# Performance work log

Measured on AMD Instinct MI355X. Metric: run time of the kernel, lower is better.

The kernel has to match this reference:

```python
import jax, jax.numpy as jnp
import numpy as np

H = 768  # sparse grid height
W = 768  # sparse grid width
N = 200000  # active sites
CIN = 256
CB = 64


def setup_inputs() -> dict:
    key = jax.random.key(0)
    ks = jax.random.split(key, 11)
    rng = np.random.default_rng(0)
    # unique active-site linear coordinates on the HxW grid
    coords = jnp.asarray(np.sort(rng.choice(H * W, N, replace=False)).astype(np.int64))
    feats = jax.random.normal(ks[0], (N, CIN), jnp.float32)
    w1 = jax.random.normal(ks[1], (CIN, CB), jnp.float32) / np.float32(np.sqrt(CIN))
    w2 = jax.random.normal(ks[2], (9, CB, CB), jnp.float32) / np.float32(np.sqrt(9 * CB))
    w3 = jax.random.normal(ks[3], (CB, CIN), jnp.float32) / np.float32(np.sqrt(CB))
    s1 = jax.random.uniform(ks[4], (CB,), jnp.float32, 0.5, 1.5)
    b1 = jax.random.normal(ks[5], (CB,), jnp.float32) * 0.1
    s2 = jax.random.uniform(ks[6], (CB,), jnp.float32, 0.5, 1.5)
    b2 = jax.random.normal(ks[7], (CB,), jnp.float32) * 0.1
    s3 = jax.random.uniform(ks[8], (CIN,), jnp.float32, 0.5, 1.5)
    b3 = jax.random.normal(ks[9], (CIN,), jnp.float32) * 0.1
    return dict(feats=feats, coords=coords, w1=w1, w2=w2, w3=w3,
                s1=s1, b1=b1, s2=s2, b2=b2, s3=s3, b3=b3)


def sparse_conv3x3(feats, coords, w2):
    # active-site sparse 3x3 conv: gather valid neighbors, matmul per tap, accumulate
    idx_map = jnp.full((H * W,), -1, jnp.int32).at[coords].set(
        jnp.arange(N, dtype=jnp.int32))
    y, x = coords // W, coords % W
    out = jnp.zeros((N, w2.shape[2]), feats.dtype)
    k = 0
    for dy in (-1, 0, 1):
        for dx in (-1, 0, 1):
            ny, nx = y + dy, x + dx
            inb = (ny >= 0) & (ny < H) & (nx >= 0) & (nx < W)
            lin = jnp.clip(ny, 0, H - 1) * W + jnp.clip(nx, 0, W - 1)
            r = idx_map[lin]
            ok = inb & (r >= 0)
            g = jnp.where(ok[:, None], feats[jnp.maximum(r, 0)], 0.0)
            out = out + g @ w2[k]
            k += 1
    return out


def reference(feats, coords, w1, w2, w3, s1, b1, s2, b2, s3, b3):
    identity = feats
    out = jax.nn.relu((feats @ w1) * s1 + b1)            # conv1 1x1 + bn1 + relu
    out = jax.nn.relu(sparse_conv3x3(out, coords, w2) * s2 + b2)  # conv2 3x3 + bn2 + relu
    out = (out @ w3) * s3 + b3                            # conv3 1x1 + bn3
    return jax.nn.relu(out + identity)                    # residual + relu
```

## Files before the change

kernel.cpp:

```cpp
#include <hip/hip_runtime.h>
#include <hip/hip_bf16.h>
#include <stdint.h>

#define HH 768
#define WW 768
#define NN 200000
#define CI 256
#define CB 64

typedef __attribute__((ext_vector_type(8))) __bf16 bf16x8;
typedef __attribute__((ext_vector_type(4))) float f32x4;

__device__ inline unsigned short f2bf(float f) {
    union { float f; unsigned int i; } v; v.f = f;
    unsigned int r = v.i + 0x7FFF + ((v.i >> 16) & 1);
    return (unsigned short)(r >> 16);
}
__device__ inline f32x4 mfma16(bf16x8 a, bf16x8 b, f32x4 c) {
    return __builtin_amdgcn_mfma_f32_16x16x32_bf16(a, b, c, 0, 0, 0);
}
__device__ inline bf16x8 ldfrag(const unsigned short* p) {
    return *(const bf16x8*)p;
}
__device__ inline bf16x8 ldfrag_f32(const float* p) {
    float4 f0 = *(const float4*)(p);
    float4 f1 = *(const float4*)(p + 4);
    bf16x8 a;
    a[0] = (__bf16)f0.x; a[1] = (__bf16)f0.y; a[2] = (__bf16)f0.z; a[3] = (__bf16)f0.w;
    a[4] = (__bf16)f1.x; a[5] = (__bf16)f1.y; a[6] = (__bf16)f1.z; a[7] = (__bf16)f1.w;
    return a;
}


__global__ void k_scatter(const int* __restrict__ coords, int* __restrict__ idx_map) {
    int i = blockIdx.x * 256 + threadIdx.x;
    if (i < NN) idx_map[coords[i]] = i;
}

__global__ void k_prepw(const float* __restrict__ w1,
                        const float* __restrict__ w2,
                        const float* __restrict__ w3,
                        unsigned short* __restrict__ w1t,
                        unsigned short* __restrict__ w2t,
                        unsigned short* __restrict__ w3t) {
    int tid = blockIdx.x * 256 + threadIdx.x;
    int stride = gridDim.x * 256;
    for (int i = tid; i < CI * CB; i += stride) {
        int k = i / CB, n = i % CB;
        w1t[n * CI + k] = f2bf(w1[i]);
    }
    for (int i = tid; i < 9 * CB * CB; i += stride) {
        int t = i / (CB * CB), rem = i % (CB * CB);
        int k = rem / CB, n = rem % CB;
        w2t[t * CB * CB + n * CB + k] = f2bf(w2[i]);
    }
    for (int i = tid; i < CB * CI; i += stride) {
        int k = i / CI, n = i % CI;
        w3t[n * CB + k] = f2bf(w3[i]);
    }
}


__global__ __launch_bounds__(256) void k_gemm1(const float* __restrict__ feats,
                                               const unsigned short* __restrict__ w1t,
                                               const float* __restrict__ s1,
                                               const float* __restrict__ b1,
                                               unsigned short* __restrict__ out1) {
    const int wave = threadIdx.x >> 6;
    const int lane = threadIdx.x & 63;
    const int m = lane & 15;
    const int quad = lane >> 4;
    const int row0 = blockIdx.x * 64 + wave * 16;
    const int row = row0 + m;

    f32x4 acc[4];
#pragma unroll
    for (int t = 0; t < 4; ++t) acc[t] = (f32x4){0.f, 0.f, 0.f, 0.f};

    const float* arow = feats + row * CI + quad * 8;
#pragma unroll
    for (int ks = 0; ks < CI / 32; ++ks) {
        bf16x8 a = ldfrag_f32(arow + ks * 32);
#pragma unroll
        for (int t = 0; t < 4; ++t) {
            bf16x8 b = ldfrag(w1t + (t * 16 + m) * CI + quad * 8 + ks * 32);
            acc[t] = mfma16(a, b, acc[t]);
        }
    }

#pragma unroll
    for (int t = 0; t < 4; ++t) {
        int col = t * 16 + m;
        float sc = s1[col], bi = b1[col];
#pragma unroll
        for (int r = 0; r < 4; ++r) {
            int orow = row0 + quad * 4 + r;
            float v = acc[t][r] * sc + bi;
            v = v > 0.f ? v : 0.f;
            out1[orow * CB + col] = f2bf(v);
        }
    }
}


__global__ __launch_bounds__(256) void k_conv(const unsigned short* __restrict__ out1,
                                              const unsigned short* __restrict__ w2t,
                                              const int* __restrict__ coords,
                                              const int* __restrict__ idx_map,
                                              const float* __restrict__ s2,
                                              const float* __restrict__ b2,
                                              unsigned short* __restrict__ out2) {
    const int wave = threadIdx.x >> 6;
    const int lane = threadIdx.x & 63;
    const int m = lane & 15;
    const int quad = lane >> 4;
    const int row0 = blockIdx.x * 64 + wave * 16;
    const int row = row0 + m;

    const int c = coords[row];
    const int y = c / WW, x = c - y * WW;

    f32x4 acc[4];
#pragma unroll
    for (int t = 0; t < 4; ++t) acc[t] = (f32x4){0.f, 0.f, 0.f, 0.f};

#pragma unroll
    for (int t = 0; t < 9; ++t) {
        const int dy = t / 3 - 1, dx = t % 3 - 1;
        const int ny = y + dy, nx = x + dx;
        int r = -1;
        if (ny >= 0 && ny < HH && nx >= 0 && nx < WW) r = idx_map[ny * WW + nx];
#pragma unroll
        for (int ks = 0; ks < 2; ++ks) {
            bf16x8 a;
#pragma unroll
            for (int j = 0; j < 8; ++j) a[j] = (__bf16)0.0f;
            if (r >= 0) a = ldfrag(out1 + r * CB + quad * 8 + ks * 32);
#pragma unroll
            for (int nt = 0; nt < 4; ++nt) {
                bf16x8 b = ldfrag(w2t + t * CB * CB + (nt * 16 + m) * CB + quad * 8 + ks * 32);
                acc[nt] = mfma16(a, b, acc[nt]);
            }
        }
    }

#pragma unroll
    for (int nt = 0; nt < 4; ++nt) {
        int col = nt * 16 + m;
        float sc = s2[col], bi = b2[col];
#pragma unroll
        for (int r = 0; r < 4; ++r) {
            int orow = row0 + quad * 4 + r;
            float v = acc[nt][r] * sc + bi;
            v = v > 0.f ? v : 0.f;
            out2[orow * CB + col] = f2bf(v);
        }
    }
}


__global__ __launch_bounds__(256) void k_gemm3(const unsigned short* __restrict__ out2,
                                               const unsigned short* __restrict__ w3t,
                                               const float* __restrict__ s3,
                                               const float* __restrict__ b3,
                                               const float* __restrict__ feats,
                                               float* __restrict__ out) {
    const int wave = threadIdx.x >> 6;
    const int lane = threadIdx.x & 63;
    const int m = lane & 15;
    const int quad = lane >> 4;
    const int row0 = blockIdx.x * 64 + wave * 16;
    const int row = row0 + m;

    f32x4 acc[16];
#pragma unroll
    for (int t = 0; t < 16; ++t) acc[t] = (f32x4){0.f, 0.f, 0.f, 0.f};

    bf16x8 a0 = ldfrag(out2 + row * CB + quad * 8);
    bf16x8 a1 = ldfrag(out2 + row * CB + quad * 8 + 32);
#pragma unroll
    for (int nt = 0; nt < 16; ++nt) {
        const unsigned short* bp = w3t + (nt * 16 + m) * CB + quad * 8;
        acc[nt] = mfma16(a0, ldfrag(bp), acc[nt]);
        acc[nt] = mfma16(a1, ldfrag(bp + 32), acc[nt]);
    }

#pragma unroll
    for (int nt = 0; nt < 16; ++nt) {
        int col = nt * 16 + m;
        float sc = s3[col], bi = b3[col];
#pragma unroll
        for (int r = 0; r < 4; ++r) {
            int orow = row0 + quad * 4 + r;
            float v = acc[nt][r] * sc + bi + feats[orow * CI + col];
            v = v > 0.f ? v : 0.f;
            out[orow * CI + col] = v;
        }
    }
}


extern "C" void kernel_launch(void* const* d_in, const int* in_sizes, int n_in,
                              void* d_out, int out_size, void* d_ws, size_t ws_size,
                              hipStream_t stream) {
    const float* feats = (const float*)d_in[0];
    const int* coords = (const int*)d_in[1];
    const float* w1 = (const float*)d_in[2];
    const float* w2 = (const float*)d_in[3];
    const float* w3 = (const float*)d_in[4];
    const float* s1 = (const float*)d_in[5];
    const float* b1 = (const float*)d_in[6];
    const float* s2 = (const float*)d_in[7];
    const float* b2 = (const float*)d_in[8];
    const float* s3 = (const float*)d_in[9];
    const float* b3 = (const float*)d_in[10];
    float* out = (float*)d_out;

    char* ws = (char*)d_ws;
    int* idx_map        = (int*)(ws + 0);
    unsigned short* w1t = (unsigned short*)(ws + 2359296);
    unsigned short* w2t = (unsigned short*)(ws + 2392064);
    unsigned short* w3t = (unsigned short*)(ws + 2465792);
    unsigned short* out1= (unsigned short*)(ws + 2498560);
    unsigned short* out2= (unsigned short*)(ws + 28098560);

    hipMemsetAsync(idx_map, 0xFF, (size_t)HH * WW * 4, stream);
    k_scatter<<<(NN + 255) / 256, 256, 0, stream>>>(coords, idx_map);
    k_prepw<<<64, 256, 0, stream>>>(w1, w2, w3, w1t, w2t, w3t);
    k_gemm1<<<NN / 64, 256, 0, stream>>>(feats, w1t, s1, b1, out1);
    k_conv<<<NN / 64, 256, 0, stream>>>(out1, w2t, coords, idx_map, s2, b2, out2);
    k_gemm3<<<NN / 64, 256, 0, stream>>>(out2, w3t, s3, b3, feats, out);
}
```

Baseline: 591.7 us.

## Register-block all three GEMM stages to 64x64 wave tiles, stage conv neighbors in LDS

Each wave now computes a 64-row by 64-column tile: four M-subtiles by four N-subtiles of MFMA accumulators. Each weight fragment load is therefore reused across four row blocks instead of one, in gemm1, conv and gemm3. The conv kernel first computes all nine neighbor indices per row into shared memory. It then gathers from a zeroed dummy row instead of branching on missing neighbors. gemm3 splits the 256 output columns across the four waves so they share the same activation rows. The trade-off is much higher register pressure, capped by launch bounds of 2 blocks per CU, and fewer waves for gemm1 and conv.

```diff
diff --git a/kernel.cpp b/kernel.cpp
--- a/kernel.cpp
+++ b/kernel.cpp
@@ -61,142 +61,186 @@
 }
 
 
-__global__ __launch_bounds__(256) void k_gemm1(const float* __restrict__ feats,
-                                               const unsigned short* __restrict__ w1t,
-                                               const float* __restrict__ s1,
-                                               const float* __restrict__ b1,
-                                               unsigned short* __restrict__ out1) {
+__global__ __launch_bounds__(256, 2) void k_gemm1(const float* __restrict__ feats,
+                                                  const unsigned short* __restrict__ w1t,
+                                                  const float* __restrict__ s1,
+                                                  const float* __restrict__ b1,
+                                                  unsigned short* __restrict__ out1) {
     const int wave = threadIdx.x >> 6;
     const int lane = threadIdx.x & 63;
     const int m = lane & 15;
     const int quad = lane >> 4;
-    const int row0 = blockIdx.x * 64 + wave * 16;
-    const int row = row0 + m;
-
-    f32x4 acc[4];
-#pragma unroll
-    for (int t = 0; t < 4; ++t) acc[t] = (f32x4){0.f, 0.f, 0.f, 0.f};
-
-    const float* arow = feats + row * CI + quad * 8;
-#pragma unroll
-    for (int ks = 0; ks < CI / 32; ++ks) {
-        bf16x8 a = ldfrag_f32(arow + ks * 32);
-#pragma unroll
-        for (int t = 0; t < 4; ++t) {
-            bf16x8 b = ldfrag(w1t + (t * 16 + m) * CI + quad * 8 + ks * 32);
-            acc[t] = mfma16(a, b, acc[t]);
-        }
-    }
-
-#pragma unroll
-    for (int t = 0; t < 4; ++t) {
-        int col = t * 16 + m;
-        float sc = s1[col], bi = b1[col];
-#pragma unroll
-        for (int r = 0; r < 4; ++r) {
-            int orow = row0 + quad * 4 + r;
-            float v = acc[t][r] * sc + bi;
-            v = v > 0.f ? v : 0.f;
-            out1[orow * CB + col] = f2bf(v);
-        }
-    }
-}
-
-
-__global__ __launch_bounds__(256) void k_conv(const unsigned short* __restrict__ out1,
-                                              const unsigned short* __restrict__ w2t,
-                                              const int* __restrict__ coords,
-                                              const int* __restrict__ idx_map,
-                                              const float* __restrict__ s2,
-                                              const float* __restrict__ b2,
-                                              unsigned short* __restrict__ out2) {
+    const int gw = blockIdx.x * 4 + wave;
+    if (gw >= NN / 64) return;
+    const int row0 = gw * 64;
+
+    f32x4 acc[4][4];
+#pragma unroll
+    for (int mt = 0; mt < 4; ++mt)
+#pragma unroll
+        for (int nt = 0; nt < 4; ++nt) acc[mt][nt] = (f32x4){0.f, 0.f, 0.f, 0.f};
+
+#pragma unroll
+    for (int ks = 0; ks < 8; ++ks) {
+        bf16x8 a[4];
+#pragma unroll
+        for (int mt = 0; mt < 4; ++mt)
+            a[mt] = ldfrag_f32(feats + (size_t)(row0 + mt * 16 + m) * CI + quad * 8 + ks * 32);
+#pragma unroll
+        for (int nt = 0; nt < 4; ++nt) {
+            bf16x8 b = ldfrag(w1t + (nt * 16 + m) * CI + quad * 8 + ks * 32);
+#pragma unroll
+            for (int mt = 0; mt < 4; ++mt)
+                acc[mt][nt] = mfma16(a[mt], b, acc[mt][nt]);
+        }
+    }
+
+#pragma unroll
+    for (int mt = 0; mt < 4; ++mt)
+#pragma unroll
+        for (int nt = 0; nt < 4; ++nt) {
+            int col = nt * 16 + m;
+            float sc = s1[col], bi = b1[col];
+#pragma unroll
+            for (int r = 0; r < 4; ++r) {
+                int orow = row0 + mt * 16 + quad * 4 + r;
+                float v = acc[mt][nt][r] * sc + bi;
+                v = v > 0.f ? v : 0.f;
+                out1[orow * CB + col] = f2bf(v);
+            }
+        }
+}
+
+
+__global__ __launch_bounds__(256, 2) void k_conv(const unsigned short* __restrict__ out1,
+                                                 const unsigned short* __restrict__ w2t,
+                                                 const int* __restrict__ coords,
+                                                 const int* __restrict__ idx_map,
+                                                 const float* __restrict__ s2,
+                                                 const float* __restrict__ b2,
+                                                 const unsigned short* __restrict__ zrow,
+                                                 unsigned short* __restrict__ out2) {
+    __shared__ int s_nbr[256 * 9];
+    const int tid = threadIdx.x;
+    const int grow = blockIdx.x * 256 + tid;
+    if (grow < NN) {
+        int c = coords[grow];
+        int y = c / WW, x = c - y * WW;
+#pragma unroll
+        for (int t = 0; t < 9; ++t) {
+            int dy = t / 3 - 1, dx = t % 3 - 1;
+            int ny = y + dy, nx = x + dx;
+            int r = -1;
+            if (ny >= 0 && ny < HH && nx >= 0 && nx < WW) r = idx_map[ny * WW + nx];
+            s_nbr[tid * 9 + t] = r;
+        }
+    } else {
+#pragma unroll
+        for (int t = 0; t < 9; ++t) s_nbr[tid * 9 + t] = -1;
+    }
+    __syncthreads();
+
+    const int wave = tid >> 6;
+    const int lane = tid & 63;
+    const int m = lane & 15;
+    const int quad = lane >> 4;
+    const int row0 = blockIdx.x * 256 + wave * 64;
+    if (row0 >= NN) return;
+
+    f32x4 acc[4][4];
+#pragma unroll
+    for (int mt = 0; mt < 4; ++mt)
+#pragma unroll
+        for (int nt = 0; nt < 4; ++nt) acc[mt][nt] = (f32x4){0.f, 0.f, 0.f, 0.f};
+
+#pragma unroll
+    for (int t = 0; t < 9; ++t) {
+        bf16x8 a[4][2];
+#pragma unroll
+        for (int mt = 0; mt < 4; ++mt) {
+            int r = s_nbr[(wave * 64 + mt * 16 + m) * 9 + t];
+            const unsigned short* base = (r >= 0) ? (out1 + (size_t)r * CB) : zrow;
+            a[mt][0] = ldfrag(base + quad * 8);
+            a[mt][1] = ldfrag(base + quad * 8 + 32);
+        }
+#pragma unroll
+        for (int ks = 0; ks < 2; ++ks)
+#pragma unroll
+            for (int nt = 0; nt < 4; ++nt) {
+                bf16x8 b = ldfrag(w2t + t * CB * CB + (nt * 16 + m) * CB + quad * 8 + ks * 32);
+#pragma unroll
+                for (int mt = 0; mt < 4; ++mt)
+                    acc[mt][nt] = mfma16(a[mt][ks], b, acc[mt][nt]);
+            }
+    }
+
+#pragma unroll
+    for (int mt = 0; mt < 4; ++mt)
+#pragma unroll
+        for (int nt = 0; nt < 4; ++nt) {
+            int col = nt * 16 + m;
+            float sc = s2[col], bi = b2[col];
+#pragma unroll
+            for (int r = 0; r < 4; ++r) {
+                int orow = row0 + mt * 16 + quad * 4 + r;
+                float v = acc[mt][nt][r] * sc + bi;
+                v = v > 0.f ? v : 0.f;
+                out2[orow * CB + col] = f2bf(v);
+            }
+        }
+}
+
+
+__global__ __launch_bounds__(256, 2) void k_gemm3(const unsigned short* __restrict__ out2,
+                                                  const unsigned short* __restrict__ w3t,
+                                                  const float* __restrict__ s3,
+                                                  const float* __restrict__ b3,
+                                                  const float* __restrict__ feats,
+                                                  float* __restrict__ out) {
     const int wave = threadIdx.x >> 6;
     const int lane = threadIdx.x & 63;
     const int m = lane & 15;
     const int quad = lane >> 4;
-    const int row0 = blockIdx.x * 64 + wave * 16;
-    const int row = row0 + m;
-
-    const int c = coords[row];
-    const int y = c / WW, x = c - y * WW;
-
-    f32x4 acc[4];
-#pragma unroll
-    for (int t = 0; t < 4; ++t) acc[t] = (f32x4){0.f, 0.f, 0.f, 0.f};
-
-#pragma unroll
-    for (int t = 0; t < 9; ++t) {
-        const int dy = t / 3 - 1, dx = t % 3 - 1;
-        const int ny = y + dy, nx = x + dx;
-        int r = -1;
-        if (ny >= 0 && ny < HH && nx >= 0 && nx < WW) r = idx_map[ny * WW + nx];
-#pragma unroll
-        for (int ks = 0; ks < 2; ++ks) {
-            bf16x8 a;
-#pragma unroll
-            for (int j = 0; j < 8; ++j) a[j] = (__bf16)0.0f;
-            if (r >= 0) a = ldfrag(out1 + r * CB + quad * 8 + ks * 32);
-#pragma unroll
-            for (int nt = 0; nt < 4; ++nt) {
-                bf16x8 b = ldfrag(w2t + t * CB * CB + (nt * 16 + m) * CB + quad * 8 + ks * 32);
-                acc[nt] = mfma16(a, b, acc[nt]);
-            }
-        }
-    }
-
-#pragma unroll
-    for (int nt = 0; nt < 4; ++nt) {
-        int col = nt * 16 + m;
-        float sc = s2[col], bi = b2[col];
-#pragma unroll
-        for (int r = 0; r < 4; ++r) {
-            int orow = row0 + quad * 4 + r;
-            float v = acc[nt][r] * sc + bi;
-            v = v > 0.f ? v : 0.f;
-            out2[orow * CB + col] = f2bf(v);
-        }
-    }
-}
-
-
-__global__ __launch_bounds__(256) void k_gemm3(const unsigned short* __restrict__ out2,
-                                               const unsigned short* __restrict__ w3t,
-                                               const float* __restrict__ s3,
-                                               const float* __restrict__ b3,
-                                               const float* __restrict__ feats,
-                                               float* __restrict__ out) {
-    const int wave = threadIdx.x >> 6;
-    const int lane = threadIdx.x & 63;
-    const int m = lane & 15;
-    const int quad = lane >> 4;
-    const int row0 = blockIdx.x * 64 + wave * 16;
-    const int row = row0 + m;
-
-    f32x4 acc[16];
-#pragma unroll
-    for (int t = 0; t < 16; ++t) acc[t] = (f32x4){0.f, 0.f, 0.f, 0.f};
-
-    bf16x8 a0 = ldfrag(out2 + row * CB + quad * 8);
-    bf16x8 a1 = ldfrag(out2 + row * CB + quad * 8 + 32);
-#pragma unroll
-    for (int nt = 0; nt < 16; ++nt) {
-        const unsigned short* bp = w3t + (nt * 16 + m) * CB + quad * 8;
-        acc[nt] = mfma16(a0, ldfrag(bp), acc[nt]);
-        acc[nt] = mfma16(a1, ldfrag(bp + 32), acc[nt]);
-    }
-
-#pragma unroll
-    for (int nt = 0; nt < 16; ++nt) {
-        int col = nt * 16 + m;
-        float sc = s3[col], bi = b3[col];
-#pragma unroll
-        for (int r = 0; r < 4; ++r) {
-            int orow = row0 + quad * 4 + r;
-            float v = acc[nt][r] * sc + bi + feats[orow * CI + col];
-            v = v > 0.f ? v : 0.f;
-            out[orow * CI + col] = v;
-        }
-    }
+    const int row0 = blockIdx.x * 64;
+    const int col0 = wave * 64;
+
+    f32x4 acc[4][4];
+#pragma unroll
+    for (int mt = 0; mt < 4; ++mt)
+#pragma unroll
+        for (int nt = 0; nt < 4; ++nt) acc[mt][nt] = (f32x4){0.f, 0.f, 0.f, 0.f};
+
+    bf16x8 a[4][2];
+#pragma unroll
+    for (int mt = 0; mt < 4; ++mt) {
+        const unsigned short* ap = out2 + (size_t)(row0 + mt * 16 + m) * CB + quad * 8;
+        a[mt][0] = ldfrag(ap);
+        a[mt][1] = ldfrag(ap + 32);
+    }
+#pragma unroll
+    for (int ks = 0; ks < 2; ++ks)
+#pragma unroll
+        for (int nt = 0; nt < 4; ++nt) {
+            bf16x8 b = ldfrag(w3t + (col0 + nt * 16 + m) * CB + quad * 8 + ks * 32);
+#pragma unroll
+            for (int mt = 0; mt < 4; ++mt)
+                acc[mt][nt] = mfma16(a[mt][ks], b, acc[mt][nt]);
+        }
+
+#pragma unroll
+    for (int mt = 0; mt < 4; ++mt)
+#pragma unroll
+        for (int nt = 0; nt < 4; ++nt) {
+            int col = col0 + nt * 16 + m;
+            float sc = s3[col], bi = b3[col];
+#pragma unroll
+            for (int r = 0; r < 4; ++r) {
+                int orow = row0 + mt * 16 + quad * 4 + r;
+                float v = acc[mt][nt][r] * sc + bi + feats[(size_t)orow * CI + col];
+                v = v > 0.f ? v : 0.f;
+                out[(size_t)orow * CI + col] = v;
+            }
+        }
 }
 
 
@@ -223,11 +267,13 @@
     unsigned short* w3t = (unsigned short*)(ws + 2465792);
     unsigned short* out1= (unsigned short*)(ws + 2498560);
     unsigned short* out2= (unsigned short*)(ws + 28098560);
+    unsigned short* zrow= (unsigned short*)(ws + 53698560);
 
     hipMemsetAsync(idx_map, 0xFF, (size_t)HH * WW * 4, stream);
+    hipMemsetAsync(zrow, 0x00, 128, stream);
     k_scatter<<<(NN + 255) / 256, 256, 0, stream>>>(coords, idx_map);
     k_prepw<<<64, 256, 0, stream>>>(w1, w2, w3, w1t, w2t, w3t);
-    k_gemm1<<<NN / 64, 256, 0, stream>>>(feats, w1t, s1, b1, out1);
-    k_conv<<<NN / 64, 256, 0, stream>>>(out1, w2t, coords, idx_map, s2, b2, out2);
+    k_gemm1<<<(NN / 64 + 3) / 4, 256, 0, stream>>>(feats, w1t, s1, b1, out1);
+    k_conv<<<(NN + 255) / 256, 256, 0, stream>>>(out1, w2t, coords, idx_map, s2, b2, zrow, out2);
     k_gemm3<<<NN / 64, 256, 0, stream>>>(out2, w3t, s3, b3, feats, out);
 }
```

New measurement: 526.6 us. 1.12x faster.
